# Kernel tuning notes

Hardware: AMD Instinct MI355X
Metric: run time of the kernel (lower is better)

## Reference

```python
import jax, jax.numpy as jnp
import numpy as np
from jax.scipy.special import logsumexp

B, T, V, D, HD, L = 64, 512, 100000, 300, 256, 9
H = HD // 2  # per-direction hidden size


def _lstm_dir(x, w_ih, w_hh, b_ih, b_hh, reverse):
    # x: [T, B, in]; PyTorch LSTM gate order: i, f, g, o
    xp = jnp.einsum('tbd,gd->tbg', x, w_ih) + b_ih + b_hh  # [T,B,4H]

    def step(carry, xt):
        h, c = carry
        g = xt + h @ w_hh.T
        i, f, gg, o = jnp.split(g, 4, axis=-1)
        c = jax.nn.sigmoid(f) * c + jax.nn.sigmoid(i) * jnp.tanh(gg)
        h = jax.nn.sigmoid(o) * jnp.tanh(c)
        return (h, c), h

    Bn = x.shape[1]
    init = (jnp.zeros((Bn, H), x.dtype), jnp.zeros((Bn, H), x.dtype))
    _, hs = jax.lax.scan(step, init, xp, reverse=reverse)
    return hs  # [T,B,H]


def _bilstm_layer(x, w_ih, w_hh, b_ih, b_hh):
    hf = _lstm_dir(x, w_ih[0], w_hh[0], b_ih[0], b_hh[0], False)
    hb = _lstm_dir(x, w_ih[1], w_hh[1], b_ih[1], b_hh[1], True)
    return jnp.concatenate([hf, hb], axis=-1)  # [T,B,2H]


def _crf_nll(em, tags, mask, start_t, end_t, trans):
    # em: [B,T,L] emissions; torchcrf log-likelihood with reduction='sum'
    mf = mask.astype(em.dtype)
    em_sel = jnp.take_along_axis(em, tags[:, :, None], axis=2)[..., 0]  # [B,T]
    num = start_t[tags[:, 0]] + em_sel[:, 0]
    tr = trans[tags[:, :-1], tags[:, 1:]]  # [B,T-1]
    num = num + ((tr + em_sel[:, 1:]) * mf[:, 1:]).sum(axis=1)
    seq_ends = mask.sum(axis=1) - 1
    last_tags = jnp.take_along_axis(tags, seq_ends[:, None], axis=1)[:, 0]
    num = num + end_t[last_tags]

    # log-partition via scan over time
    alpha0 = start_t[None, :] + em[:, 0]  # [B,L]

    def step(alpha, inp):
        em_t, m_t = inp  # [B,L], [B]
        nxt = logsumexp(alpha[:, :, None] + trans[None] + em_t[:, None, :], axis=1)
        return jnp.where(m_t[:, None], nxt, alpha), None

    alpha, _ = jax.lax.scan(step, alpha0,
                            (em[:, 1:].transpose(1, 0, 2), mask[:, 1:].T))
    denom = logsumexp(alpha + end_t[None, :], axis=1)
    llh = (num - denom).sum()
    return -llh  # model returns -loss (NLL)


def setup_inputs() -> dict:
    key = jax.random.key(0)
    ks = jax.random.split(key, 18)
    w = lambda k, s: jax.random.normal(k, s, dtype=jnp.float32) * 0.08
    inp = {
        'word_batch': jax.random.randint(ks[0], (B, T), 1, V),  # >=1 so mask is all-true
        'label_batch': jax.random.randint(ks[1], (B, T), 0, L),
        'emb': jax.random.normal(ks[2], (V, D), dtype=jnp.float32) * 0.1,
        'w_ih_l0': w(ks[3], (2, 4 * H, D)),
        'w_hh_l0': w(ks[4], (2, 4 * H, H)),
        'b_ih_l0': w(ks[5], (2, 4 * H)),
        'b_hh_l0': w(ks[6], (2, 4 * H)),
        'w_ih_l1': w(ks[7], (2, 4 * H, HD)),
        'w_hh_l1': w(ks[8], (2, 4 * H, H)),
        'b_ih_l1': w(ks[9], (2, 4 * H)),
        'b_hh_l1': w(ks[10], (2, 4 * H)),
        'w_out': w(ks[11], (L, HD)),
        'b_out': w(ks[12], (L,)),
        'start_t': w(ks[13], (L,)),
        'end_t': w(ks[14], (L,)),
        'trans': w(ks[15], (L, L)),
    }
    return inp


def reference(word_batch, label_batch, emb,
              w_ih_l0, w_hh_l0, b_ih_l0, b_hh_l0,
              w_ih_l1, w_hh_l1, b_ih_l1, b_hh_l1,
              w_out, b_out, start_t, end_t, trans):
    mask = word_batch > 0  # [B,T], all-true by construction
    x = emb[word_batch].transpose(1, 0, 2)  # [T,B,D] (dropout is eval no-op)
    x = _bilstm_layer(x, w_ih_l0, w_hh_l0, b_ih_l0, b_hh_l0)
    x = _bilstm_layer(x, w_ih_l1, w_hh_l1, b_ih_l1, b_hh_l1)
    em = jnp.einsum('tbh,lh->btl', x, w_out) + b_out  # [B,T,L]
    return _crf_nll(em, label_batch, mask, start_t, end_t, trans)
```

## Files before the change

### kernel.cpp

```cpp
#include <hip/hip_runtime.h>

#define TT 512
#define NB 64
#define HH 128
#define G4 512
#define HDIM 256

typedef __bf16 bf16x8 __attribute__((ext_vector_type(8)));
typedef float f32x4 __attribute__((ext_vector_type(4)));
typedef float f32x2 __attribute__((ext_vector_type(2)));
typedef unsigned int u32x4 __attribute__((ext_vector_type(4)));
typedef unsigned int u32x2 __attribute__((ext_vector_type(2)));

union FragU { u32x4 u4; bf16x8 bf; unsigned short us[8]; };
union XPU { u32x2 v; unsigned short us[4]; };

#define SC_SIG  -1.442695041f
#define SC_TANH -2.885390082f

__device__ __forceinline__ unsigned short f2bf(float f){
  unsigned u = __builtin_bit_cast(unsigned, f);
  return (unsigned short)((u + 0x7FFFu + ((u>>16)&1u)) >> 16);
}
__device__ __forceinline__ float bf2f(unsigned short h){
  unsigned u = ((unsigned)h) << 16;
  return __builtin_bit_cast(float, u);
}
__device__ __forceinline__ float rsig(float y){
  return __builtin_amdgcn_rcpf(1.0f + __builtin_amdgcn_exp2f(y));
}


__global__ __launch_bounds__(256) void k_prep(
    const float* __restrict__ bi0, const float* __restrict__ bh0,
    const float* __restrict__ bi1, const float* __restrict__ bh1,
    const float* __restrict__ w_ih0, const float* __restrict__ w_ih1,
    float* __restrict__ bias0, float* __restrict__ bias1,
    unsigned short* __restrict__ Bp0, unsigned short* __restrict__ Bp1)
{
  int id = blockIdx.x*256 + threadIdx.x;
  if (id < 2048){
    int n = id & 511;
    float s = ((n >> 7) == 2) ? SC_TANH : SC_SIG;
    if (id < 1024) bias0[id] = (bi0[id] + bh0[id]) * s;
    else { int k = id - 1024; bias1[k] = (bi1[k] + bh1[k]) * s; }
    return;
  }
  id -= 2048;
  if (id < 320*1024){
    int k = id >> 10, c = id & 1023;
    int dir = c >> 9, n = c & 511;
    float s = ((n >> 7) == 2) ? SC_TANH : SC_SIG;
    float v = (k < 300) ? w_ih0[((size_t)(dir*512 + n))*300 + k] * s : 0.f;
    Bp0[(((size_t)(k>>3))*1024 + c)*8 + (k&7)] = f2bf(v);
    return;
  }
  id -= 320*1024;
  if (id < 256*1024){
    int k = id >> 10, c = id & 1023;
    int dir = c >> 9, n = c & 511;
    float s = ((n >> 7) == 2) ? SC_TANH : SC_SIG;
    float v = w_ih1[((size_t)(dir*512 + n))*256 + k] * s;
    Bp1[(((size_t)(k>>3))*1024 + c)*8 + (k&7)] = f2bf(v);
  }
}

__global__ __launch_bounds__(320) void k_embed(
    const int* __restrict__ word, const float* __restrict__ emb,
    unsigned short* __restrict__ xe)
{
  int row = blockIdx.x;
  int c = threadIdx.x;
  int t = row >> 6, b = row & 63;
  int wd = word[b*TT + t];
  float v = (c < 300) ? emb[(size_t)wd*300 + c] : 0.f;
  xe[(size_t)row*320 + c] = f2bf(v);
}


__global__ __launch_bounds__(256) void k_gemm(
    const unsigned short* __restrict__ A,
    const unsigned short* __restrict__ Bp,
    const float* __restrict__ bias,
    unsigned short* __restrict__ xp,
    const int lda, const int KB)
{
  const int tid = threadIdx.x;
  const int l = tid & 63, w = tid >> 6;
  const int quad = l >> 4, lo = l & 15;
  const int wm = w >> 1, wn = w & 1;
  const int M0 = blockIdx.x * 128;
  const int N0 = blockIdx.y * 128;

  __shared__ __align__(16) unsigned short Asl[4*128*8];
  __shared__ __align__(16) unsigned short Bsl[4*128*8];

  f32x4 acc[4][4] = {};

  for (int kb=0; kb<KB; ++kb){
    const int k0 = kb*32;
    u32x4 va[2], vb[2];
    #pragma unroll
    for (int hh=0; hh<2; ++hh){
      const int cch = tid + hh*256;
      const int q = cch >> 7, mm = cch & 127;
      va[hh] = *(const u32x4*)(A + (size_t)(M0+mm)*lda + k0 + q*8);
      vb[hh] = *(const u32x4*)(Bp + (((size_t)((k0>>3)+q))*1024 + N0 + mm)*8);
    }
    __syncthreads();
    #pragma unroll
    for (int hh=0; hh<2; ++hh){
      const int cch = tid + hh*256;
      *(u32x4*)&Asl[cch*8] = va[hh];
      *(u32x4*)&Bsl[cch*8] = vb[hh];
    }
    __syncthreads();

    FragU af[4], bfg[4];
    #pragma unroll
    for (int mt=0; mt<4; ++mt)
      af[mt].u4 = *(const u32x4*)&Asl[((quad<<7) + wm*64 + mt*16 + lo)*8];
    #pragma unroll
    for (int nt=0; nt<4; ++nt)
      bfg[nt].u4 = *(const u32x4*)&Bsl[((quad<<7) + wn*64 + nt*16 + lo)*8];
    #pragma unroll
    for (int mt=0; mt<4; ++mt)
      #pragma unroll
      for (int nt=0; nt<4; ++nt)
        acc[mt][nt] = __builtin_amdgcn_mfma_f32_16x16x32_bf16(af[mt].bf, bfg[nt].bf, acc[mt][nt], 0, 0, 0);
  }

  #pragma unroll
  for (int mt=0; mt<4; ++mt){
    #pragma unroll
    for (int nt=0; nt<4; ++nt){
      const int col = N0 + wn*64 + nt*16 + lo;
      const int dir = col >> 9, n = col & 511;
      const float bv = bias[col];
      const int g  = n >> 7;
      const int u  = n & 127;
      const int wS = u >> 5;
      const int lS0 = (u & 31) * 2;
      #pragma unroll
      for (int r=0; r<4; ++r){
        const int row = M0 + wm*64 + mt*16 + quad*4 + r;
        const int t = row >> 6, b = row & 63;
        const int bidS = dir*32 + (b >> 1);
        const int lS = lS0 + (b & 1);
        const size_t o = ((((size_t)bidS*TT + t)*4 + wS)*64 + lS)*4 + g;
        xp[o] = f2bf(acc[mt][nt][r] + bv);
      }
    }
  }
}


__global__ __launch_bounds__(256, 1) void k_scan(
    const float* __restrict__ w_hh,
    const unsigned short* __restrict__ xp,
    unsigned short* __restrict__ xout)
{
  const int bid = blockIdx.x;
  const int dir = bid >> 5, bg = bid & 31;
  const int tid = threadIdx.x;
  const int l = tid & 63, w = tid >> 6;
  const int quad = l >> 4, lo = l & 15;
  const int up = l >> 1;
  const int b  = l & 1;

  FragU bw[8][4];
  {
    const float* wb = w_hh + (size_t)dir*G4*HH;
    #pragma unroll
    for (int nt=0; nt<8; ++nt){
      const int g = nt >> 1;
      const float s = (g == 2) ? SC_TANH : SC_SIG;
      const int grow = g*HH + w*32 + (nt&1)*16 + lo;
      #pragma unroll
      for (int kq=0; kq<4; ++kq){
        const float* p = wb + (size_t)grow*HH + kq*32 + quad*8;
        #pragma unroll
        for (int j=0; j<8; ++j) bw[nt][kq].us[j] = f2bf(p[j] * s);
      }
    }
  }

  __shared__ __align__(16) unsigned short hbuf[2][16][136];
  __shared__ __align__(16) float scr[4][4][16][4];
  for (int i = tid; i < 2*16*136; i += 256) ((unsigned short*)hbuf)[i] = 0;
  __syncthreads();

  float c = 0.f;
  const int t0 = dir ? (TT-1) : 0;
  const int dt = dir ? -1 : 1;
  const unsigned short* xpb = xp + (((size_t)bid*TT*4 + w)*64 + l)*4;

  u32x2 pf[4];
  #pragma unroll
  for (int k=0; k<4; ++k)
    pf[k] = *(const u32x2*)(xpb + (size_t)(t0 + dt*k)*1024);

  const f32x4 zero4 = {0.f, 0.f, 0.f, 0.f};

  for (int ob=0; ob<TT/4; ++ob){
    #pragma unroll
    for (int ph=0; ph<4; ++ph){
      const int it = ob*4 + ph;
      const int t = t0 + dt*it;
      const int rb = ph & 1;
      const int wb2 = rb ^ 1;

      FragU af[4];
      #pragma unroll
      for (int kq=0; kq<4; ++kq)
        af[kq].u4 = *(const u32x4*)&hbuf[rb][lo][kq*32 + quad*8];

      f32x4 acc[8];
      #pragma unroll
      for (int nt=0; nt<8; ++nt)
        acc[nt] = __builtin_amdgcn_mfma_f32_16x16x32_bf16(af[0].bf, bw[nt][0].bf, zero4, 0, 0, 0);
      #pragma unroll
      for (int kq=1; kq<4; ++kq)
        #pragma unroll
        for (int nt=0; nt<8; ++nt)
          acc[nt] = __builtin_amdgcn_mfma_f32_16x16x32_bf16(af[kq].bf, bw[nt][kq].bf, acc[nt], 0, 0, 0);

      XPU xu; xu.v = pf[ph];
      {
        const int itp = (it+4 < TT) ? (it+4) : (TT-1);
        pf[ph] = *(const u32x2*)(xpb + (size_t)(t0 + dt*itp)*1024);
      }

      if (quad == 0){
        #pragma unroll
        for (int g=0; g<4; ++g){
          *(f32x2*)&scr[w][g][lo][0] = *(const f32x2*)&acc[g*2];
          *(f32x2*)&scr[w][g][lo][2] = *(const f32x2*)&acc[g*2+1];
        }
      }
      float gv[4];
      #pragma unroll
      for (int g=0; g<4; ++g)
        gv[g] = scr[w][g][up & 15][((up >> 4) << 1) | b] + bf2f(xu.us[g]);

      float si = rsig(gv[0]), sf = rsig(gv[1]);
      float tg = __builtin_fmaf(2.0f, rsig(gv[2]), -1.0f);
      float so = rsig(gv[3]);
      c = __builtin_fmaf(sf, c, si*tg);
      float h = so * __builtin_fmaf(2.0f, rsig(SC_TANH*c), -1.0f);
      unsigned short hb = f2bf(h);
      hbuf[wb2][b][w*32 + up] = hb;
      xout[((size_t)t*NB + bg*2 + b)*HDIM + dir*HH + w*32 + up] = hb;

      asm volatile("s_waitcnt lgkmcnt(0)\n\ts_barrier" ::: "memory");
    }
  }
}


__global__ __launch_bounds__(256) void k_em(
    const unsigned short* __restrict__ x2,
    const float* __restrict__ w_out,
    const float* __restrict__ b_out,
    float* __restrict__ em)
{
  const int tid = threadIdx.x;
  const int l = tid & 63, w = tid >> 6;
  const int quad = l >> 4, lo = l & 15;
  const int M0 = blockIdx.x*128 + w*32;

  FragU bf[8];
  #pragma unroll
  for (int kq=0; kq<8; ++kq){
    #pragma unroll
    for (int j=0; j<8; ++j){
      float v = (lo < 9) ? w_out[lo*HDIM + kq*32 + quad*8 + j] : 0.f;
      bf[kq].us[j] = f2bf(v);
    }
  }

  f32x4 acc[2] = {};
  #pragma unroll
  for (int kq=0; kq<8; ++kq){
    FragU a0, a1;
    a0.u4 = *(const u32x4*)(x2 + ((size_t)(M0 + lo))*HDIM + kq*32 + quad*8);
    a1.u4 = *(const u32x4*)(x2 + ((size_t)(M0 + 16 + lo))*HDIM + kq*32 + quad*8);
    acc[0] = __builtin_amdgcn_mfma_f32_16x16x32_bf16(a0.bf, bf[kq].bf, acc[0], 0, 0, 0);
    acc[1] = __builtin_amdgcn_mfma_f32_16x16x32_bf16(a1.bf, bf[kq].bf, acc[1], 0, 0, 0);
  }

  if (lo < 9){
    const float bo = b_out[lo];
    #pragma unroll
    for (int mt=0; mt<2; ++mt){
      #pragma unroll
      for (int r=0; r<4; ++r){
        const int row = M0 + mt*16 + quad*4 + r;
        const int t = row >> 6, b = row & 63;
        em[((size_t)b*TT + t)*9 + lo] = acc[mt][r] + bo;
      }
    }
  }
}


__global__ __launch_bounds__(128) void k_crf_r1f(
    const int* __restrict__ word, const float* __restrict__ em,
    const float* __restrict__ start_t, const float* __restrict__ trans,
    float* __restrict__ dst)
{
  const int bid = blockIdx.x;
  const int b = bid >> 6, g = bid & 63;
  const int tid = threadIdx.x;
  const int t0 = g*8;
  __shared__ float R[2][81];
  __shared__ float emsh[8][9];
  __shared__ int wsh[8];
  if (tid < 72){
    int s = tid/9, j = tid - (tid/9)*9;
    emsh[s][j] = em[((size_t)b*TT + t0+s)*9 + j];
  }
  if (tid < 8) wsh[tid] = word[b*TT + t0 + tid];
  __syncthreads();
  int i=0, j=0; float tr[9];
  if (tid < 81){
    i = tid/9; j = tid - i*9;
    #pragma unroll
    for (int k=0;k<9;++k) tr[k] = trans[k*9+j];
    float v;
    if (t0 == 0) v = start_t[j] + emsh[0][j];
    else if (wsh[0] > 0) v = tr[i] + emsh[0][j];
    else v = (i==j) ? 0.f : -1e30f;
    R[0][tid] = v;
  }
  int cur = 0;
  for (int s=1; s<8; ++s){
    __syncthreads();
    if (tid < 81){
      if (wsh[s] > 0){
        float a[9], mx = -3.0e38f;
        #pragma unroll
        for (int k=0;k<9;++k){ a[k] = R[cur][i*9+k] + tr[k]; mx = fmaxf(mx, a[k]); }
        float sm = 0.f;
        #pragma unroll
        for (int k=0;k<9;++k) sm += __expf(a[k]-mx);
        R[cur^1][tid] = mx + __logf(sm) + emsh[s][j];
      } else {
        R[cur^1][tid] = R[cur][tid];
      }
    }
    cur ^= 1;
  }
  __syncthreads();
  if (tid < 81) dst[((size_t)bid)*81 + tid] = R[cur][tid];
}

__global__ __launch_bounds__(128) void k_crf_reduce(
    const float* __restrict__ src, float* __restrict__ dst, const int nm)
{
  const int bid = blockIdx.x;
  const int ng = nm >> 3;
  const int b = bid / ng, g = bid - b*ng;
  const int tid = threadIdx.x;
  __shared__ float R[2][81];
  const float* base = src + ((size_t)b*nm + g*8)*81;
  if (tid < 81) R[0][tid] = base[tid];
  int cur = 0;
  for (int s=1; s<8; ++s){
    __syncthreads();
    if (tid < 81){
      int i = tid/9, j = tid - (tid/9)*9;
      const float* M = base + (size_t)s*81;
      float a[9], mx = -3.0e38f;
      #pragma unroll
      for (int k=0;k<9;++k){ a[k] = R[cur][i*9+k] + M[k*9+j]; mx = fmaxf(mx, a[k]); }
      float sm = 0.f;
      #pragma unroll
      for (int k=0;k<9;++k) sm += __expf(a[k]-mx);
      R[cur^1][tid] = mx + __logf(sm);
    }
    cur ^= 1;
  }
  __syncthreads();
  if (tid < 81) dst[((size_t)b*ng + g)*81 + tid] = R[cur][tid];
}

__global__ __launch_bounds__(256) void k_crf_num(
    const int* __restrict__ word, const int* __restrict__ label,
    const float* __restrict__ em, const float* __restrict__ start_t,
    const float* __restrict__ end_t, const float* __restrict__ trans,
    float* __restrict__ numv)
{
  const int b = blockIdx.x, tid = threadIdx.x;
  __shared__ float sred[256];
  __shared__ int ssend;
  int ms = 0;
  for (int t=tid; t<TT; t+=256) ms += (word[b*TT+t] > 0) ? 1 : 0;
  sred[tid] = (float)ms;
  __syncthreads();
  for (int st=128; st>0; st>>=1){ if (tid<st) sred[tid] += sred[tid+st]; __syncthreads(); }
  if (tid==0) ssend = (int)sred[0] - 1;
  __syncthreads();
  const int send = ssend;
  float part = 0.f;
  for (int t=tid; t<TT; t+=256){
    int tag = label[b*TT+t];
    float es = em[((size_t)b*TT+t)*9 + tag];
    if (t == 0) part += start_t[tag] + es;
    else if (word[b*TT+t] > 0) part += trans[label[b*TT+t-1]*9 + tag] + es;
    if (t == send) part += end_t[tag];
  }
  __syncthreads();
  sred[tid] = part;
  __syncthreads();
  for (int st=128; st>0; st>>=1){ if (tid<st) sred[tid] += sred[tid+st]; __syncthreads(); }
  if (tid==0) numv[b] = sred[0];
}

__global__ __launch_bounds__(64) void k_final(
    const float* __restrict__ numv, const float* __restrict__ G3,
    const float* __restrict__ end_t, float* __restrict__ out)
{
  const int b = threadIdx.x;
  float a[9], mx = -3.0e38f;
  #pragma unroll
  for (int j=0;j<9;++j){ a[j] = G3[b*81 + j] + end_t[j]; mx = fmaxf(mx, a[j]); }
  float sm = 0.f;
  #pragma unroll
  for (int j=0;j<9;++j) sm += __expf(a[j]-mx);
  float denom = mx + __logf(sm);
  float v = numv[b] - denom;
  #pragma unroll
  for (int off=32; off>0; off>>=1) v += __shfl_down(v, off, 64);
  if (b == 0) out[0] = -v;
}


extern "C" void kernel_launch(void* const* d_in, const int* in_sizes, int n_in,
                              void* d_out, int out_size, void* d_ws, size_t ws_size,
                              hipStream_t stream)
{
  (void)in_sizes; (void)n_in; (void)out_size; (void)ws_size;
  const int*   word  = (const int*)d_in[0];
  const int*   label = (const int*)d_in[1];
  const float* emb   = (const float*)d_in[2];
  const float* w_ih0 = (const float*)d_in[3];
  const float* w_hh0 = (const float*)d_in[4];
  const float* b_ih0 = (const float*)d_in[5];
  const float* b_hh0 = (const float*)d_in[6];
  const float* w_ih1 = (const float*)d_in[7];
  const float* w_hh1 = (const float*)d_in[8];
  const float* b_ih1 = (const float*)d_in[9];
  const float* b_hh1 = (const float*)d_in[10];
  const float* w_out = (const float*)d_in[11];
  const float* b_out = (const float*)d_in[12];
  const float* start_t = (const float*)d_in[13];
  const float* end_t   = (const float*)d_in[14];
  const float* trans   = (const float*)d_in[15];

  char* ws = (char*)d_ws;
  unsigned short* xp    = (unsigned short*)(ws + 0);
  unsigned short* xe    = (unsigned short*)(ws + 67108864);
  unsigned short* x1    = (unsigned short*)(ws + 88080384);
  unsigned short* x2    = (unsigned short*)(ws + 104857600);
  unsigned short* Bp0   = (unsigned short*)(ws + 121634816);
  unsigned short* Bp1   = (unsigned short*)(ws + 122290176);
  float*          bias0 = (float*)(ws + 122814464);
  float*          bias1 = (float*)(ws + 122818560);
  float*          em    = (float*)(ws + 122822656);
  float*          G1    = (float*)(ws + 124002304);
  float*          G2    = (float*)(ws + 125329408);
  float*          G3    = (float*)(ws + 125495296);
  float*          numv  = (float*)(ws + 125516032);

  hipLaunchKernelGGL(k_prep, dim3(2312), dim3(256), 0, stream,
                     b_ih0, b_hh0, b_ih1, b_hh1, w_ih0, w_ih1, bias0, bias1, Bp0, Bp1);
  hipLaunchKernelGGL(k_embed, dim3(32768), dim3(320), 0, stream, word, emb, xe);
  hipLaunchKernelGGL(k_gemm, dim3(256, 8), dim3(256), 0, stream, xe, Bp0, bias0, xp, 320, 10);
  hipLaunchKernelGGL(k_scan, dim3(64), dim3(256), 0, stream, w_hh0, xp, x1);
  hipLaunchKernelGGL(k_gemm, dim3(256, 8), dim3(256), 0, stream, x1, Bp1, bias1, xp, 256, 8);
  hipLaunchKernelGGL(k_scan, dim3(64), dim3(256), 0, stream, w_hh1, xp, x2);
  hipLaunchKernelGGL(k_em, dim3(256), dim3(256), 0, stream, x2, w_out, b_out, em);
  hipLaunchKernelGGL(k_crf_r1f, dim3(4096), dim3(128), 0, stream, word, em, start_t, trans, G1);
  hipLaunchKernelGGL(k_crf_reduce, dim3(512), dim3(128), 0, stream, G1, G2, 64);
  hipLaunchKernelGGL(k_crf_reduce, dim3(64), dim3(128), 0, stream, G2, G3, 8);
  hipLaunchKernelGGL(k_crf_num, dim3(64), dim3(256), 0, stream, word, label, em, start_t, end_t, trans, numv);
  hipLaunchKernelGGL(k_final, dim3(1), dim3(64), 0, stream, numv, G3, end_t, (float*)d_out);
}
```

Before: 1.003 ms.

## Read gate results directly from MFMA accumulators, dropping LDS scratch exchange

The recurrent scan kernel now maps each lane to a (batch, unit) pair that matches where the MFMA accumulator already holds its gate values. This removes the per-step LDS scratch write/read round trip, cutting LDS traffic on the serial critical path. The xp projection layout is simplified to a plain [row][dir][unit][gate] order to suit the new lane mapping, and the h buffer shrinks to only the two live batch rows. The new xp layout gives less coalesced prefetch loads with a large stride.

```diff
diff --git a/kernel.cpp b/kernel.cpp
--- a/kernel.cpp
+++ b/kernel.cpp
@@ -8,7 +8,6 @@
 
 typedef __bf16 bf16x8 __attribute__((ext_vector_type(8)));
 typedef float f32x4 __attribute__((ext_vector_type(4)));
-typedef float f32x2 __attribute__((ext_vector_type(2)));
 typedef unsigned int u32x4 __attribute__((ext_vector_type(4)));
 typedef unsigned int u32x2 __attribute__((ext_vector_type(2)));
 
@@ -136,18 +135,12 @@
     for (int nt=0; nt<4; ++nt){
       const int col = N0 + wn*64 + nt*16 + lo;
       const int dir = col >> 9, n = col & 511;
+      const int g = n >> 7, u = n & 127;
       const float bv = bias[col];
-      const int g  = n >> 7;
-      const int u  = n & 127;
-      const int wS = u >> 5;
-      const int lS0 = (u & 31) * 2;
       #pragma unroll
       for (int r=0; r<4; ++r){
         const int row = M0 + wm*64 + mt*16 + quad*4 + r;
-        const int t = row >> 6, b = row & 63;
-        const int bidS = dir*32 + (b >> 1);
-        const int lS = lS0 + (b & 1);
-        const size_t o = ((((size_t)bidS*TT + t)*4 + wS)*64 + lS)*4 + g;
+        const size_t o = (size_t)row*1024 + dir*512 + u*4 + g;
         xp[o] = f2bf(acc[mt][nt][r] + bv);
       }
     }
@@ -165,8 +158,10 @@
   const int tid = threadIdx.x;
   const int l = tid & 63, w = tid >> 6;
   const int quad = l >> 4, lo = l & 15;
-  const int up = l >> 1;
-  const int b  = l & 1;
+  const int qb = quad & 1;
+  const int qh = quad >> 1;
+  const int uu = w*32 + qh*16 + lo;
+  const int bglob = bg*2 + qb;
 
   FragU bw[8][4];
   {
@@ -185,20 +180,20 @@
     }
   }
 
-  __shared__ __align__(16) unsigned short hbuf[2][16][136];
-  __shared__ __align__(16) float scr[4][4][16][4];
-  for (int i = tid; i < 2*16*136; i += 256) ((unsigned short*)hbuf)[i] = 0;
+  __shared__ __align__(16) unsigned short hbuf[2][2][160];
+  for (int i = tid; i < 2*2*160; i += 256) ((unsigned short*)hbuf)[i] = 0;
   __syncthreads();
 
   float c = 0.f;
   const int t0 = dir ? (TT-1) : 0;
   const int dt = dir ? -1 : 1;
-  const unsigned short* xpb = xp + (((size_t)bid*TT*4 + w)*64 + l)*4;
+  const unsigned short* xpb = xp + (size_t)bglob*1024 + dir*512 + uu*4;
+  unsigned short* xob = xout + (size_t)bglob*HDIM + dir*HH + uu;
 
   u32x2 pf[4];
   #pragma unroll
   for (int k=0; k<4; ++k)
-    pf[k] = *(const u32x2*)(xpb + (size_t)(t0 + dt*k)*1024);
+    pf[k] = *(const u32x2*)(xpb + (size_t)(t0 + dt*k)*65536);
 
   const f32x4 zero4 = {0.f, 0.f, 0.f, 0.f};
 
@@ -213,7 +208,7 @@
       FragU af[4];
       #pragma unroll
       for (int kq=0; kq<4; ++kq)
-        af[kq].u4 = *(const u32x4*)&hbuf[rb][lo][kq*32 + quad*8];
+        af[kq].u4 = *(const u32x4*)&hbuf[rb][lo & 1][kq*32 + quad*8];
 
       f32x4 acc[8];
       #pragma unroll
@@ -228,20 +223,16 @@
       XPU xu; xu.v = pf[ph];
       {
         const int itp = (it+4 < TT) ? (it+4) : (TT-1);
-        pf[ph] = *(const u32x2*)(xpb + (size_t)(t0 + dt*itp)*1024);
-      }
-
-      if (quad == 0){
-        #pragma unroll
-        for (int g=0; g<4; ++g){
-          *(f32x2*)&scr[w][g][lo][0] = *(const f32x2*)&acc[g*2];
-          *(f32x2*)&scr[w][g][lo][2] = *(const f32x2*)&acc[g*2+1];
-        }
-      }
+        pf[ph] = *(const u32x2*)(xpb + (size_t)(t0 + dt*itp)*65536);
+      }
+
       float gv[4];
       #pragma unroll
-      for (int g=0; g<4; ++g)
-        gv[g] = scr[w][g][up & 15][((up >> 4) << 1) | b] + bf2f(xu.us[g]);
+      for (int g=0; g<4; ++g){
+        float ta = qb ? acc[g*2  ][1] : acc[g*2  ][0];
+        float tb = qb ? acc[g*2+1][1] : acc[g*2+1][0];
+        gv[g] = (qh ? tb : ta) + bf2f(xu.us[g]);
+      }
 
       float si = rsig(gv[0]), sf = rsig(gv[1]);
       float tg = __builtin_fmaf(2.0f, rsig(gv[2]), -1.0f);
@@ -249,8 +240,8 @@
       c = __builtin_fmaf(sf, c, si*tg);
       float h = so * __builtin_fmaf(2.0f, rsig(SC_TANH*c), -1.0f);
       unsigned short hb = f2bf(h);
-      hbuf[wb2][b][w*32 + up] = hb;
-      xout[((size_t)t*NB + bg*2 + b)*HDIM + dir*HH + w*32 + up] = hb;
+      hbuf[wb2][qb][uu] = hb;
+      xob[(size_t)t*NB*HDIM] = hb;
 
       asm volatile("s_waitcnt lgkmcnt(0)\n\ts_barrier" ::: "memory");
     }
```

Result: faster. 874.6 us (-12.8%).
